# Optimization experiments

Hardware: AMD Instinct MI355X
Metric: run time of the kernel (lower is better)

Reference implementation:

```python
import jax, jax.numpy as jnp
import numpy as np

B, W, F = 32, 100, 128   # batch, window_size, n_features
KSIZE = 7                # conv kernel size
EMB = 8                  # embedding dim for feature-similarity matrix
ALPHA = 0.2              # leaky relu negative slope


def setup_inputs() -> dict:
    key = jax.random.key(0)
    ks = jax.random.split(key, 10)
    s = 0.05
    return {
        "x": jax.random.normal(ks[0], (B, W, F), jnp.float32),
        # ConvLayer: Conv1d(F, F, KSIZE) with 'same' padding
        "conv_w": jax.random.normal(ks[1], (F, F, KSIZE), jnp.float32) * s,
        "conv_b": jnp.zeros((F,), jnp.float32),
        # TemporalAttentionLayer (GATv2): lin(2F -> 2F), a (2F,1), bias (W,W)
        "temp_lin_w": jax.random.normal(ks[2], (2 * F, 2 * F), jnp.float32) * s,
        "temp_lin_b": jnp.zeros((2 * F,), jnp.float32),
        "temp_a": jax.random.normal(ks[3], (2 * F, 1), jnp.float32) * s,
        "temp_bias": jnp.zeros((W, W), jnp.float32),
        # FeatureAttentionLayer (GATv2): lin(2W -> 2W), a (2W,1), bias (F,F)
        "feat_lin_w": jax.random.normal(ks[4], (2 * W, 2 * W), jnp.float32) * s,
        "feat_lin_b": jnp.zeros((2 * W,), jnp.float32),
        "feat_a": jax.random.normal(ks[5], (2 * W, 1), jnp.float32) * s,
        "feat_bias": jnp.zeros((F, F), jnp.float32),
        # nn.Embedding(F, EMB) table (indexed by arange(F) -> just the table)
        "emb": jax.random.normal(ks[6], (F, EMB), jnp.float32),
        # forecasting model: Linear(W, 1) + tanh
        "fc_w": jax.random.normal(ks[7], (1, W), jnp.float32) * s,
        "fc_b": jnp.zeros((1,), jnp.float32),
    }


def _pos_encode(x):
    # pe = sin(pos*div) + cos(pos*div), div = exp(arange(F) * -ln(1e4)/F)
    pos = jnp.arange(W, dtype=jnp.float32)[:, None]
    div = jnp.exp(jnp.arange(F, dtype=jnp.float32) * (-np.log(10000.0) / F))
    pe = jnp.sin(pos * div) + jnp.cos(pos * div)  # (W, F)
    return x + pe[None]


def _conv(x, w, b):
    # x: (B, W, F) -> Conv1d over time with channels = features, 'same' length
    xc = x.transpose(0, 2, 1)  # (B, F, W)
    pad = (KSIZE - 1) // 2
    y = jax.lax.conv_general_dilated(
        xc, w, window_strides=(1,), padding=[(pad, pad)],
        dimension_numbers=("NCW", "OIW", "NCW"))
    y = jax.nn.relu(y + b[None, :, None])
    return y.transpose(0, 2, 1)  # (B, W, F)


def _gat_v2(v, lin_w, lin_b, a, bias):
    # v: (B, K, D). Equivalent to lin(concat(v_i, v_j)) via split weights +
    # broadcast add (avoids the O(K^2) concat materialization).
    D = v.shape[-1]
    left = v @ lin_w[:, :D].T    # (B, K, E) -- v_i part
    right = v @ lin_w[:, D:].T   # (B, K, E) -- v_j part
    s = left[:, :, None, :] + right[:, None, :, :] + lin_b  # (B, K, K, E)
    s = jnp.where(s >= 0, s, ALPHA * s)  # leaky relu
    e = jnp.einsum("bije,e->bij", s, a[:, 0]) + bias  # (B, K, K)
    att = jax.nn.softmax(e, axis=2)
    return jnp.tanh(jnp.einsum("bij,bjd->bid", att, v))


def reference(x, conv_w, conv_b, temp_lin_w, temp_lin_b, temp_a, temp_bias,
              feat_lin_w, feat_lin_b, feat_a, feat_bias, emb, fc_w, fc_b):
    x = _pos_encode(x)                 # (B, W, F)
    x = _conv(x, conv_w, conv_b)       # (B, W, F)
    # temporal attention: nodes = time steps
    x = _gat_v2(x, temp_lin_w, temp_lin_b, temp_a, temp_bias)  # (B, W, F)
    # feature attention: nodes = features
    xf = x.transpose(0, 2, 1)          # (B, F, W)
    xf = _gat_v2(xf, feat_lin_w, feat_lin_b, feat_a, feat_bias)
    x = xf.transpose(0, 2, 1)          # (B, W, F)
    # cosine-similarity mixing over features
    norms = jnp.linalg.norm(emb, axis=-1)
    cos = (emb @ emb.T) / (norms[:, None] * norms[None, :])  # (F, F)
    x = x @ cos.T                      # (B, W, F)
    xp = x.transpose(0, 2, 1)          # (B, F, W)
    pred = jnp.tanh(xp @ fc_w.T + fc_b)  # (B, F, 1)
    return pred.transpose(0, 2, 1)     # (B, 1, F)
```

## Files before the change

### kernel.cpp

```cpp
#include <hip/hip_runtime.h>
#include <math.h>

#define BB 32
#define WW 100
#define FF 128
#define KS 7
#define ET 256
#define EF 200


__global__ void k_prep(const float* __restrict__ cw, const float* __restrict__ tlw,
                       const float* __restrict__ flw, float* __restrict__ wt,
                       float* __restrict__ tlwT, float* __restrict__ flwT) {
    int id = blockIdx.x * 256 + threadIdx.x;
    if (id < KS * FF * FF) {
        int o = id & (FF - 1);
        int r = id >> 7;
        int k = r % KS;
        int i = r / KS;
        wt[id] = cw[(o * FF + i) * KS + k];
    }
    if (id < ET * ET) {
        int e = id & (ET - 1);
        int d = id >> 8;
        tlwT[id] = tlw[e * ET + d];
    }
    if (id < EF * EF) {
        int e = id % EF;
        int d = id / EF;
        flwT[id] = flw[e * EF + d];
    }
}

#define CTW 10
#define NROW 16
#define XPAD 20
__global__ __launch_bounds__(512) void k_conv(const float* __restrict__ x,
                                              const float* __restrict__ wt,
                                              const float* __restrict__ cb,
                                              float* __restrict__ x2) {
    int b = blockIdx.x & 31;
    int tile = blockIdx.x >> 5;
    int w0 = tile * CTW;
    int tid = threadIdx.x;
    int o = tid & (FF - 1);
    int h = tid >> 7;
    __shared__ float xs[FF][XPAD];
    __shared__ float part[4][CTW][FF];
    for (int idx = tid; idx < NROW * FF; idx += 512) {
        int r = idx >> 7, f = idx & (FF - 1);
        int t = w0 - 3 + r;
        float v = 0.f;
        if ((unsigned)t < WW) {
            float div = __expf((float)f * (-9.210340371976184f / (float)FF));
            float arg = (float)t * div;
            v = x[(b * WW + t) * FF + f] + __sinf(arg) + __cosf(arg);
        }
        xs[f][r] = v;
    }
    __syncthreads();
    float acc[CTW];
#pragma unroll
    for (int t = 0; t < CTW; ++t) acc[t] = 0.f;
    const float* wbase = wt + (h * 32) * KS * FF + o;
#pragma unroll 2
    for (int il = 0; il < 32; ++il) {
        int i = h * 32 + il;
        float4 X0 = *(const float4*)&xs[i][0];
        float4 X1 = *(const float4*)&xs[i][4];
        float4 X2 = *(const float4*)&xs[i][8];
        float4 X3 = *(const float4*)&xs[i][12];
        float xr[16] = {X0.x, X0.y, X0.z, X0.w, X1.x, X1.y, X1.z, X1.w,
                        X2.x, X2.y, X2.z, X2.w, X3.x, X3.y, X3.z, X3.w};
        const float* wp = wbase + il * KS * FF;
#pragma unroll
        for (int k = 0; k < KS; ++k) {
            float wv = wp[k * FF];
#pragma unroll
            for (int t = 0; t < CTW; ++t) acc[t] += xr[t + k] * wv;
        }
    }
#pragma unroll
    for (int t = 0; t < CTW; ++t) part[h][t][o] = acc[t];
    __syncthreads();
    for (int idx = tid; idx < CTW * FF; idx += 512) {
        int t = idx >> 7, oo = idx & (FF - 1);
        float s = part[0][t][oo] + part[1][t][oo] + part[2][t][oo] +
                  part[3][t][oo] + cb[oo];
        x2[(b * WW + w0 + t) * FF + oo] = fmaxf(s, 0.f);
    }
}

__global__ __launch_bounds__(512) void k_lr_t(const float* __restrict__ x2,
                                              const float* __restrict__ tlwT,
                                              const float* __restrict__ tlb,
                                              float* __restrict__ LT,
                                              float* __restrict__ Rt) {
    int b = blockIdx.x & 31;
    int tile = blockIdx.x >> 5;
    int i0 = tile * 8;
    int tid = threadIdx.x;
    int e = tid & 255;
    int rh = tid >> 8;
    __shared__ float xs[8][FF];
    for (int idx = tid; idx < 8 * FF; idx += 512) {
        int r = idx >> 7, d = idx & (FF - 1);
        int row = i0 + r; if (row >= WW) row = WW - 1;
        xs[r][d] = x2[(b * WW + row) * FF + d];
    }
    __syncthreads();
    float aL[4] = {0, 0, 0, 0}, aR[4] = {0, 0, 0, 0};
    const float* wl = tlwT + e;
#pragma unroll 2
    for (int dc = 0; dc < 32; ++dc) {
        float xv[4][4];
#pragma unroll
        for (int r = 0; r < 4; ++r)
            *(float4*)xv[r] = *(const float4*)&xs[rh * 4 + r][dc * 4];
#pragma unroll
        for (int q = 0; q < 4; ++q) {
            int d = dc * 4 + q;
            float wL = wl[d * ET];
            float wR = wl[(FF + d) * ET];
#pragma unroll
            for (int r = 0; r < 4; ++r) {
                aL[r] += xv[r][q] * wL;
                aR[r] += xv[r][q] * wR;
            }
        }
    }
    int ibase = i0 + rh * 4;
    if (ibase < WW) {
        float lb = tlb[e];
        float o0[4];
#pragma unroll
        for (int r = 0; r < 4; ++r) o0[r] = aL[r] + lb;
        *(float4*)&LT[(b * ET + e) * WW + ibase] = *(float4*)o0;
        *(float4*)&Rt[(b * ET + e) * WW + ibase] = *(float4*)aR;
    }
}

__global__ __launch_bounds__(512) void k_att_t(const float* __restrict__ LT,
                                               const float* __restrict__ Rt,
                                               const float* __restrict__ ta,
                                               const float* __restrict__ tbias,
                                               const float* __restrict__ x2,
                                               float* __restrict__ x3T) {
    int b = blockIdx.x & 31;
    int tile = blockIdx.x >> 5;
    int i0 = tile * 8;
    int tid = threadIdx.x;
    int j = tid & 127, g = tid >> 7;
    __shared__ float Rs[2][32][FF];
    __shared__ float Ls[2][32][8];
    __shared__ float tas[ET];
    __shared__ float attQ[8][FF];
    __shared__ float ob[8][FF];
    __shared__ float redA[8][2], redB[8][2];
    if (tid < ET) tas[tid] = ta[tid];

    float rv[8];
    float lvr = 0.f;
    {
        const float* Rb = Rt + (b * ET) * WW;
#pragma unroll
        for (int it = 0; it < 8; ++it) {
            int idx = tid + it * 512;
            int er = idx >> 7, w = idx & 127;
            rv[it] = (w < WW) ? Rb[er * WW + w] : 0.f;
        }
        if (tid < 256) {
            int er = tid >> 3, qq = tid & 7;
            int row = i0 + qq; if (row >= WW) row = WW - 1;
            lvr = LT[(b * ET + er) * WW + row];
        }
    }
#pragma unroll
    for (int it = 0; it < 8; ++it) {
        int idx = tid + it * 512;
        Rs[0][idx >> 7][idx & 127] = rv[it];
    }
    if (tid < 256) Ls[0][tid >> 3][tid & 7] = lvr;
    __syncthreads();

    float s0 = 0.f, s1 = 0.f;
    for (int ch = 0; ch < 8; ++ch) {
        int buf = ch & 1;
        if (ch < 7) {
            int e0 = (ch + 1) * 32;
            const float* Rb = Rt + (b * ET + e0) * WW;
#pragma unroll
            for (int it = 0; it < 8; ++it) {
                int idx = tid + it * 512;
                int er = idx >> 7, w = idx & 127;
                rv[it] = (w < WW) ? Rb[er * WW + w] : 0.f;
            }
            if (tid < 256) {
                int er = tid >> 3, qq = tid & 7;
                int row = i0 + qq; if (row >= WW) row = WW - 1;
                lvr = LT[(b * ET + e0 + er) * WW + row];
            }
        }
        int e0 = ch * 32;
#pragma unroll 8
        for (int e = 0; e < 32; ++e) {
            float rj = Rs[buf][e][j];
            float ae = tas[e0 + e];
            float2 lv2 = *(const float2*)&Ls[buf][e][g * 2];
            float v;
            v = lv2.x + rj; v = fmaxf(v, 0.2f * v); s0 += v * ae;
            v = lv2.y + rj; v = fmaxf(v, 0.2f * v); s1 += v * ae;
        }
        if (ch < 7) {
#pragma unroll
            for (int it = 0; it < 8; ++it) {
                int idx = tid + it * 512;
                Rs[buf ^ 1][idx >> 7][idx & 127] = rv[it];
            }
            if (tid < 256) Ls[buf ^ 1][tid >> 3][tid & 7] = lvr;
        }
        __syncthreads();
    }

    float ej[2];
    {
        int iq = i0 + g * 2;
        float bv0 = (j < WW && iq < WW) ? tbias[iq * WW + j] : 0.f;
        float bv1 = (j < WW && iq + 1 < WW) ? tbias[(iq + 1) * WW + j] : 0.f;
        ej[0] = (j < WW && iq < WW) ? s0 + bv0 : -1e30f;
        ej[1] = (j < WW && iq + 1 < WW) ? s1 + bv1 : -1e30f;
    }
    float m[2] = {ej[0], ej[1]};
#pragma unroll
    for (int off = 32; off > 0; off >>= 1) {
#pragma unroll
        for (int ii = 0; ii < 2; ++ii) m[ii] = fmaxf(m[ii], __shfl_xor(m[ii], off));
    }
    int wv = tid >> 6;
    if ((tid & 63) == 0) { redA[wv][0] = m[0]; redA[wv][1] = m[1]; }
    __syncthreads();
    float p[2], ps[2];
#pragma unroll
    for (int ii = 0; ii < 2; ++ii) {
        float mx = fmaxf(redA[g * 2][ii], redA[g * 2 + 1][ii]);
        p[ii] = (j < WW) ? __expf(ej[ii] - mx) : 0.f;
        ps[ii] = p[ii];
    }
#pragma unroll
    for (int off = 32; off > 0; off >>= 1) {
#pragma unroll
        for (int ii = 0; ii < 2; ++ii) ps[ii] += __shfl_xor(ps[ii], off);
    }
    if ((tid & 63) == 0) { redB[wv][0] = ps[0]; redB[wv][1] = ps[1]; }
    __syncthreads();
#pragma unroll
    for (int ii = 0; ii < 2; ++ii) {
        float inv = 1.f / (redB[g * 2][ii] + redB[g * 2 + 1][ii]);
        attQ[g * 2 + ii][j] = p[ii] * inv;
    }

    int d = j, ph = g;
    float pv0 = 0.f, pv1 = 0.f;
#pragma unroll
    for (int it = 0; it < 8; ++it) {
        int idx = tid + it * 512;
        int r = idx >> 7, f = idx & 127;
        rv[it] = (r < WW) ? x2[(b * WW + r) * FF + f] : 0.f;
    }
    __syncthreads();
#pragma unroll
    for (int it = 0; it < 8; ++it) {
        int idx = tid + it * 512;
        Rs[0][idx >> 7][idx & 127] = rv[it];
    }
    __syncthreads();
    const float* a0 = attQ[ph * 2];
    const float* a1 = attQ[ph * 2 + 1];
    for (int jc = 0; jc < 4; ++jc) {
        int buf = jc & 1;
        if (jc < 3) {
            int r0 = (jc + 1) * 32;
#pragma unroll
            for (int it = 0; it < 8; ++it) {
                int idx = tid + it * 512;
                int r = idx >> 7, f = idx & 127;
                int row = r0 + r;
                rv[it] = (row < WW) ? x2[(b * WW + row) * FF + f] : 0.f;
            }
        }
#pragma unroll 8
        for (int r = 0; r < 32; ++r) {
            float xv = Rs[buf][r][d];
            int row = jc * 32 + r;
            pv0 += a0[row] * xv;
            pv1 += a1[row] * xv;
        }
        if (jc < 3) {
#pragma unroll
            for (int it = 0; it < 8; ++it) {
                int idx = tid + it * 512;
                Rs[buf ^ 1][idx >> 7][idx & 127] = rv[it];
            }
        }
        __syncthreads();
    }
    ob[ph * 2][d] = tanhf(pv0);
    ob[ph * 2 + 1][d] = tanhf(pv1);
    __syncthreads();
    if (tid < 256) {
        int f = tid >> 1, half = tid & 1;
        if (i0 + half * 4 < WW) {
            float4 v = make_float4(ob[half * 4][f], ob[half * 4 + 1][f],
                                   ob[half * 4 + 2][f], ob[half * 4 + 3][f]);
            *(float4*)&x3T[(b * FF + f) * WW + i0 + half * 4] = v;
        }
    }
}

__global__ __launch_bounds__(512) void k_lr_f(const float* __restrict__ x3T,
                                              const float* __restrict__ flwT,
                                              const float* __restrict__ flb,
                                              float* __restrict__ LfT,
                                              float* __restrict__ RfT) {
    int b = blockIdx.x & 31;
    int tile = blockIdx.x >> 5;
    int f0 = tile * 8;
    int tid = threadIdx.x;
    int e = tid & 255;
    int rh = tid >> 8;
    __shared__ float xs[8][WW];
    for (int idx = tid; idx < 8 * WW; idx += 512) {
        int r = idx / WW, d = idx % WW;
        xs[r][d] = x3T[(b * FF + f0 + r) * WW + d];
    }
    __syncthreads();
    if (e < EF) {
        float aL[4] = {0, 0, 0, 0}, aR[4] = {0, 0, 0, 0};
        const float* wl = flwT + e;
#pragma unroll 2
        for (int dc = 0; dc < 25; ++dc) {
            float xv[4][4];
#pragma unroll
            for (int r = 0; r < 4; ++r)
                *(float4*)xv[r] = *(const float4*)&xs[rh * 4 + r][dc * 4];
#pragma unroll
            for (int q = 0; q < 4; ++q) {
                int d = dc * 4 + q;
                float wL = wl[d * EF];
                float wR = wl[(WW + d) * EF];
#pragma unroll
                for (int r = 0; r < 4; ++r) {
                    aL[r] += xv[r][q] * wL;
                    aR[r] += xv[r][q] * wR;
                }
            }
        }
        float lb = flb[e];
        float o0[4];
#pragma unroll
        for (int r = 0; r < 4; ++r) o0[r] = aL[r] + lb;
        int fbase = f0 + rh * 4;
        *(float4*)&LfT[(b * EF + e) * FF + fbase] = *(float4*)o0;
        *(float4*)&RfT[(b * EF + e) * FF + fbase] = *(float4*)aR;
    }
}

__global__ __launch_bounds__(512) void k_att_f(const float* __restrict__ LfT,
                                               const float* __restrict__ RfT,
                                               const float* __restrict__ fa,
                                               const float* __restrict__ fbias,
                                               const float* __restrict__ x3T,
                                               const float* __restrict__ fcw,
                                               float* __restrict__ tj) {
    int b = blockIdx.x & 31;
    int tile = blockIdx.x >> 5;
    int f0 = tile * 8;
    int tid = threadIdx.x;
    int j = tid & 127, g = tid >> 7;
    __shared__ float Rs[2][40][FF];
    __shared__ float Ls[2][40][8];
    __shared__ float fas[EF];
    __shared__ float attQ[8][FF];
    __shared__ float redA[8][2], redB[8][2], redT[8][2];
    if (tid < EF) fas[tid] = fa[tid];

    float rv[10];
    float lvr = 0.f;
    {
        const float* Rb = RfT + (b * EF) * FF;
#pragma unroll
        for (int it = 0; it < 10; ++it) {
            int idx = tid + it * 512;
            rv[it] = Rb[idx];
        }
        if (tid < 320) {
            int er = tid >> 3, qq = tid & 7;
            lvr = LfT[(b * EF + er) * FF + f0 + qq];
        }
    }
#pragma unroll
    for (int it = 0; it < 10; ++it) {
        int idx = tid + it * 512;
        Rs[0][idx >> 7][idx & 127] = rv[it];
    }
    if (tid < 320) Ls[0][tid >> 3][tid & 7] = lvr;
    __syncthreads();

    float s0 = 0.f, s1 = 0.f;
    for (int ch = 0; ch < 5; ++ch) {
        int buf = ch & 1;
        if (ch < 4) {
            int e0 = (ch + 1) * 40;
            const float* Rb = RfT + (b * EF + e0) * FF;
#pragma unroll
            for (int it = 0; it < 10; ++it) {
                int idx = tid + it * 512;
                rv[it] = Rb[idx];
            }
            if (tid < 320) {
                int er = tid >> 3, qq = tid & 7;
                lvr = LfT[(b * EF + e0 + er) * FF + f0 + qq];
            }
        }
        int e0 = ch * 40;
#pragma unroll 8
        for (int e = 0; e < 40; ++e) {
            float rj = Rs[buf][e][j];
            float ae = fas[e0 + e];
            float2 lv2 = *(const float2*)&Ls[buf][e][g * 2];
            float v;
            v = lv2.x + rj; v = fmaxf(v, 0.2f * v); s0 += v * ae;
            v = lv2.y + rj; v = fmaxf(v, 0.2f * v); s1 += v * ae;
        }
        if (ch < 4) {
#pragma unroll
            for (int it = 0; it < 10; ++it) {
                int idx = tid + it * 512;
                Rs[buf ^ 1][idx >> 7][idx & 127] = rv[it];
            }
            if (tid < 320) Ls[buf ^ 1][tid >> 3][tid & 7] = lvr;
        }
        __syncthreads();
    }

    float ej[2] = {s0 + fbias[(f0 + g * 2) * FF + j],
                   s1 + fbias[(f0 + g * 2 + 1) * FF + j]};
    float m[2] = {ej[0], ej[1]};
#pragma unroll
    for (int off = 32; off > 0; off >>= 1) {
#pragma unroll
        for (int ii = 0; ii < 2; ++ii) m[ii] = fmaxf(m[ii], __shfl_xor(m[ii], off));
    }
    int wv = tid >> 6;
    if ((tid & 63) == 0) { redA[wv][0] = m[0]; redA[wv][1] = m[1]; }
    __syncthreads();
    float p[2], ps[2];
#pragma unroll
    for (int ii = 0; ii < 2; ++ii) {
        float mx = fmaxf(redA[g * 2][ii], redA[g * 2 + 1][ii]);
        p[ii] = __expf(ej[ii] - mx);
        ps[ii] = p[ii];
    }
#pragma unroll
    for (int off = 32; off > 0; off >>= 1) {
#pragma unroll
        for (int ii = 0; ii < 2; ++ii) ps[ii] += __shfl_xor(ps[ii], off);
    }
    if ((tid & 63) == 0) { redB[wv][0] = ps[0]; redB[wv][1] = ps[1]; }
    __syncthreads();
#pragma unroll
    for (int ii = 0; ii < 2; ++ii) {
        float inv = 1.f / (redB[g * 2][ii] + redB[g * 2 + 1][ii]);
        attQ[g * 2 + ii][j] = p[ii] * inv;
    }

    int w = j, ph = g;
    float pv0 = 0.f, pv1 = 0.f;
#pragma unroll
    for (int it = 0; it < 8; ++it) {
        int idx = tid + it * 512;
        int r = idx >> 7, ww = idx & 127;
        rv[it] = (ww < WW) ? x3T[(b * FF + r) * WW + ww] : 0.f;
    }
    __syncthreads();
#pragma unroll
    for (int it = 0; it < 8; ++it) {
        int idx = tid + it * 512;
        Rs[0][idx >> 7][idx & 127] = rv[it];
    }
    __syncthreads();
    const float* a0 = attQ[ph * 2];
    const float* a1 = attQ[ph * 2 + 1];
    for (int jc = 0; jc < 4; ++jc) {
        int buf = jc & 1;
        if (jc < 3) {
            int r0 = (jc + 1) * 32;
#pragma unroll
            for (int it = 0; it < 8; ++it) {
                int idx = tid + it * 512;
                int r = idx >> 7, ww = idx & 127;
                rv[it] = (ww < WW) ? x3T[(b * FF + r0 + r) * WW + ww] : 0.f;
            }
        }
#pragma unroll 8
        for (int r = 0; r < 32; ++r) {
            float xv = Rs[buf][r][w];
            int row = jc * 32 + r;
            pv0 += a0[row] * xv;
            pv1 += a1[row] * xv;
        }
        if (jc < 3) {
#pragma unroll
            for (int it = 0; it < 8; ++it) {
                int idx = tid + it * 512;
                Rs[buf ^ 1][idx >> 7][idx & 127] = rv[it];
            }
        }
        __syncthreads();
    }
    bool wok = (w < WW);
    float fcv = wok ? fcw[w] : 0.f;
    float tv[2] = {tanhf(pv0) * fcv, tanhf(pv1) * fcv};
#pragma unroll
    for (int off = 32; off > 0; off >>= 1) {
#pragma unroll
        for (int ii = 0; ii < 2; ++ii) tv[ii] += __shfl_xor(tv[ii], off);
    }
    if ((tid & 63) == 0) { redT[wv][0] = tv[0]; redT[wv][1] = tv[1]; }
    __syncthreads();
    if (tid < 8) {
        int q = tid, php = q >> 1, ii = q & 1;
        tj[b * FF + f0 + q] = redT[php * 2][ii] + redT[php * 2 + 1][ii];
    }
}

__global__ __launch_bounds__(128) void k_fc(const float* __restrict__ tjg,
                                            const float* __restrict__ emb,
                                            const float* __restrict__ fcb,
                                            float* __restrict__ out) {
    int b = blockIdx.x;
    int f = threadIdx.x;
    __shared__ float en[FF][12];
    __shared__ float tjs[FF];
    {
        float4 e0 = *(const float4*)&emb[f * 8];
        float4 e1 = *(const float4*)&emb[f * 8 + 4];
        float n = e0.x*e0.x + e0.y*e0.y + e0.z*e0.z + e0.w*e0.w +
                  e1.x*e1.x + e1.y*e1.y + e1.z*e1.z + e1.w*e1.w;
        float rin = rsqrtf(n);
        float4 a = make_float4(e0.x*rin, e0.y*rin, e0.z*rin, e0.w*rin);
        float4 c = make_float4(e1.x*rin, e1.y*rin, e1.z*rin, e1.w*rin);
        *(float4*)&en[f][0] = a;
        *(float4*)&en[f][4] = c;
        tjs[f] = tjg[b * FF + f];
    }
    __syncthreads();
    float er[8];
#pragma unroll
    for (int k = 0; k < 8; ++k) er[k] = en[f][k];
    float acc = fcb[0];
    for (int jj = 0; jj < FF; ++jj) {
        float4 a = *(const float4*)&en[jj][0];
        float4 c = *(const float4*)&en[jj][4];
        float d8 = er[0]*a.x + er[1]*a.y + er[2]*a.z + er[3]*a.w +
                   er[4]*c.x + er[5]*c.y + er[6]*c.z + er[7]*c.w;
        acc += d8 * tjs[jj];
    }
    out[b * FF + f] = tanhf(acc);
}

extern "C" void kernel_launch(void* const* d_in, const int* in_sizes, int n_in,
                              void* d_out, int out_size, void* d_ws, size_t ws_size,
                              hipStream_t stream) {
    const float* x     = (const float*)d_in[0];
    const float* cw    = (const float*)d_in[1];
    const float* cb    = (const float*)d_in[2];
    const float* tlw   = (const float*)d_in[3];
    const float* tlb   = (const float*)d_in[4];
    const float* ta    = (const float*)d_in[5];
    const float* tbias = (const float*)d_in[6];
    const float* flw   = (const float*)d_in[7];
    const float* flb   = (const float*)d_in[8];
    const float* fa    = (const float*)d_in[9];
    const float* fbias = (const float*)d_in[10];
    const float* emb   = (const float*)d_in[11];
    const float* fcw   = (const float*)d_in[12];
    const float* fcb   = (const float*)d_in[13];
    float* out = (float*)d_out;
    float* ws = (float*)d_ws;

    float* x2   = ws + 409600;
    float* x3T  = ws + 819200;
    float* LT   = ws + 1228800;
    float* Rt   = ws + 2048000;
    float* tj   = ws + 2867200;
    float* wt   = ws + 3297280;
    float* tlwT = ws + 3411968;
    float* flwT = ws + 3477504;

    k_prep<<<448, 256, 0, stream>>>(cw, tlw, flw, wt, tlwT, flwT);
    k_conv<<<BB * 10, 512, 0, stream>>>(x, wt, cb, x2);
    k_lr_t<<<BB * 13, 512, 0, stream>>>(x2, tlwT, tlb, LT, Rt);
    k_att_t<<<BB * 13, 512, 0, stream>>>(LT, Rt, ta, tbias, x2, x3T);
    k_lr_f<<<BB * 16, 512, 0, stream>>>(x3T, flwT, flb, LT, Rt);
    k_att_f<<<BB * 16, 512, 0, stream>>>(LT, Rt, fa, fbias, x3T, fcw, tj);
    k_fc<<<BB, 128, 0, stream>>>(tj, emb, fcb, out);
}
```

Baseline: 118.2 us.

## Fuse temporal linear projection into conv and final FC into feature attention

The temporal GAT linear projection (L/R) is computed inside the conv kernel from the conv output held in shared memory, so the separate k_lr_t launch and its reload of x2 go away. The final cosine-mixing FC step moves into k_att_f: an atomic per-batch counter, reset in k_prep, picks the last finishing block for each batch, and that block computes the output. This saves two kernel launches and some global traffic. In exchange the conv kernel does more work per block at 320 blocks, and the result relies on threadfence/atomic ordering.

```diff
diff --git a/kernel.cpp b/kernel.cpp
--- a/kernel.cpp
+++ b/kernel.cpp
@@ -11,8 +11,10 @@
 
 __global__ void k_prep(const float* __restrict__ cw, const float* __restrict__ tlw,
                        const float* __restrict__ flw, float* __restrict__ wt,
-                       float* __restrict__ tlwT, float* __restrict__ flwT) {
+                       float* __restrict__ tlwT, float* __restrict__ flwT,
+                       int* __restrict__ cnt) {
     int id = blockIdx.x * 256 + threadIdx.x;
+    if (id < 32) cnt[id] = 0;
     if (id < KS * FF * FF) {
         int o = id & (FF - 1);
         int r = id >> 7;
@@ -38,7 +40,11 @@
 __global__ __launch_bounds__(512) void k_conv(const float* __restrict__ x,
                                               const float* __restrict__ wt,
                                               const float* __restrict__ cb,
-                                              float* __restrict__ x2) {
+                                              const float* __restrict__ tlwT,
+                                              const float* __restrict__ tlb,
+                                              float* __restrict__ x2,
+                                              float* __restrict__ LT,
+                                              float* __restrict__ Rt) {
     int b = blockIdx.x & 31;
     int tile = blockIdx.x >> 5;
     int w0 = tile * CTW;
@@ -47,6 +53,7 @@
     int h = tid >> 7;
     __shared__ float xs[FF][XPAD];
     __shared__ float part[4][CTW][FF];
+    __shared__ float xs2[CTW][FF];
     for (int idx = tid; idx < NROW * FF; idx += 512) {
         int r = idx >> 7, f = idx & (FF - 1);
         int t = w0 - 3 + r;
@@ -87,56 +94,41 @@
         int t = idx >> 7, oo = idx & (FF - 1);
         float s = part[0][t][oo] + part[1][t][oo] + part[2][t][oo] +
                   part[3][t][oo] + cb[oo];
-        x2[(b * WW + w0 + t) * FF + oo] = fmaxf(s, 0.f);
-    }
-}
-
-__global__ __launch_bounds__(512) void k_lr_t(const float* __restrict__ x2,
-                                              const float* __restrict__ tlwT,
-                                              const float* __restrict__ tlb,
-                                              float* __restrict__ LT,
-                                              float* __restrict__ Rt) {
-    int b = blockIdx.x & 31;
-    int tile = blockIdx.x >> 5;
-    int i0 = tile * 8;
-    int tid = threadIdx.x;
+        s = fmaxf(s, 0.f);
+        x2[(b * WW + w0 + t) * FF + oo] = s;
+        xs2[t][oo] = s;
+    }
+    __syncthreads();
     int e = tid & 255;
     int rh = tid >> 8;
-    __shared__ float xs[8][FF];
-    for (int idx = tid; idx < 8 * FF; idx += 512) {
-        int r = idx >> 7, d = idx & (FF - 1);
-        int row = i0 + r; if (row >= WW) row = WW - 1;
-        xs[r][d] = x2[(b * WW + row) * FF + d];
-    }
-    __syncthreads();
-    float aL[4] = {0, 0, 0, 0}, aR[4] = {0, 0, 0, 0};
+    float aL[5] = {0, 0, 0, 0, 0}, aR[5] = {0, 0, 0, 0, 0};
     const float* wl = tlwT + e;
 #pragma unroll 2
     for (int dc = 0; dc < 32; ++dc) {
-        float xv[4][4];
-#pragma unroll
-        for (int r = 0; r < 4; ++r)
-            *(float4*)xv[r] = *(const float4*)&xs[rh * 4 + r][dc * 4];
+        float xv[5][4];
+#pragma unroll
+        for (int r = 0; r < 5; ++r)
+            *(float4*)xv[r] = *(const float4*)&xs2[rh * 5 + r][dc * 4];
 #pragma unroll
         for (int q = 0; q < 4; ++q) {
             int d = dc * 4 + q;
             float wL = wl[d * ET];
             float wR = wl[(FF + d) * ET];
 #pragma unroll
-            for (int r = 0; r < 4; ++r) {
+            for (int r = 0; r < 5; ++r) {
                 aL[r] += xv[r][q] * wL;
                 aR[r] += xv[r][q] * wR;
             }
         }
     }
-    int ibase = i0 + rh * 4;
-    if (ibase < WW) {
-        float lb = tlb[e];
-        float o0[4];
-#pragma unroll
-        for (int r = 0; r < 4; ++r) o0[r] = aL[r] + lb;
-        *(float4*)&LT[(b * ET + e) * WW + ibase] = *(float4*)o0;
-        *(float4*)&Rt[(b * ET + e) * WW + ibase] = *(float4*)aR;
+    float lb = tlb[e];
+    int ibase = w0 + rh * 5;
+    float* Lp = LT + (b * ET + e) * WW + ibase;
+    float* Rp = Rt + (b * ET + e) * WW + ibase;
+#pragma unroll
+    for (int r = 0; r < 5; ++r) {
+        Lp[r] = aL[r] + lb;
+        Rp[r] = aR[r];
     }
 }
 
@@ -371,7 +363,11 @@
                                                const float* __restrict__ fbias,
                                                const float* __restrict__ x3T,
                                                const float* __restrict__ fcw,
-                                               float* __restrict__ tj) {
+                                               const float* __restrict__ emb,
+                                               const float* __restrict__ fcb,
+                                               float* __restrict__ tj,
+                                               int* __restrict__ cnt,
+                                               float* __restrict__ out) {
     int b = blockIdx.x & 31;
     int tile = blockIdx.x >> 5;
     int f0 = tile * 8;
@@ -382,6 +378,9 @@
     __shared__ float fas[EF];
     __shared__ float attQ[8][FF];
     __shared__ float redA[8][2], redB[8][2], redT[8][2];
+    __shared__ float en[FF][12];
+    __shared__ float tjs2[FF];
+    __shared__ int isLast;
     if (tid < EF) fas[tid] = fa[tid];
 
     float rv[10];
@@ -532,41 +531,45 @@
         int q = tid, php = q >> 1, ii = q & 1;
         tj[b * FF + f0 + q] = redT[php * 2][ii] + redT[php * 2 + 1][ii];
     }
-}
-
-__global__ __launch_bounds__(128) void k_fc(const float* __restrict__ tjg,
-                                            const float* __restrict__ emb,
-                                            const float* __restrict__ fcb,
-                                            float* __restrict__ out) {
-    int b = blockIdx.x;
-    int f = threadIdx.x;
-    __shared__ float en[FF][12];
-    __shared__ float tjs[FF];
-    {
-        float4 e0 = *(const float4*)&emb[f * 8];
-        float4 e1 = *(const float4*)&emb[f * 8 + 4];
-        float n = e0.x*e0.x + e0.y*e0.y + e0.z*e0.z + e0.w*e0.w +
-                  e1.x*e1.x + e1.y*e1.y + e1.z*e1.z + e1.w*e1.w;
-        float rin = rsqrtf(n);
-        float4 a = make_float4(e0.x*rin, e0.y*rin, e0.z*rin, e0.w*rin);
-        float4 c = make_float4(e1.x*rin, e1.y*rin, e1.z*rin, e1.w*rin);
-        *(float4*)&en[f][0] = a;
-        *(float4*)&en[f][4] = c;
-        tjs[f] = tjg[b * FF + f];
-    }
-    __syncthreads();
-    float er[8];
-#pragma unroll
-    for (int k = 0; k < 8; ++k) er[k] = en[f][k];
-    float acc = fcb[0];
-    for (int jj = 0; jj < FF; ++jj) {
-        float4 a = *(const float4*)&en[jj][0];
-        float4 c = *(const float4*)&en[jj][4];
-        float d8 = er[0]*a.x + er[1]*a.y + er[2]*a.z + er[3]*a.w +
-                   er[4]*c.x + er[5]*c.y + er[6]*c.z + er[7]*c.w;
-        acc += d8 * tjs[jj];
-    }
-    out[b * FF + f] = tanhf(acc);
+    __syncthreads();
+    if (tid == 0) {
+        __threadfence();
+        int old = atomicAdd(&cnt[b], 1);
+        isLast = (old == 15);
+    }
+    __syncthreads();
+    if (isLast) {
+        __threadfence();
+        if (tid < 128) {
+            int f = tid;
+            float4 e0 = *(const float4*)&emb[f * 8];
+            float4 e1 = *(const float4*)&emb[f * 8 + 4];
+            float n = e0.x*e0.x + e0.y*e0.y + e0.z*e0.z + e0.w*e0.w +
+                      e1.x*e1.x + e1.y*e1.y + e1.z*e1.z + e1.w*e1.w;
+            float rin = rsqrtf(n);
+            en[f][0] = e0.x*rin; en[f][1] = e0.y*rin;
+            en[f][2] = e0.z*rin; en[f][3] = e0.w*rin;
+            en[f][4] = e1.x*rin; en[f][5] = e1.y*rin;
+            en[f][6] = e1.z*rin; en[f][7] = e1.w*rin;
+            tjs2[f] = tj[b * FF + f];
+        }
+        __syncthreads();
+        if (tid < 128) {
+            int f = tid;
+            float er[8];
+#pragma unroll
+            for (int k = 0; k < 8; ++k) er[k] = en[f][k];
+            float acc = fcb[0];
+            for (int jj = 0; jj < FF; ++jj) {
+                float4 a = *(const float4*)&en[jj][0];
+                float4 c = *(const float4*)&en[jj][4];
+                float d8 = er[0]*a.x + er[1]*a.y + er[2]*a.z + er[3]*a.w +
+                           er[4]*c.x + er[5]*c.y + er[6]*c.z + er[7]*c.w;
+                acc += d8 * tjs2[jj];
+            }
+            out[b * FF + f] = tanhf(acc);
+        }
+    }
 }
 
 extern "C" void kernel_launch(void* const* d_in, const int* in_sizes, int n_in,
@@ -594,15 +597,15 @@
     float* LT   = ws + 1228800;
     float* Rt   = ws + 2048000;
     float* tj   = ws + 2867200;
+    int*   cnt  = (int*)(ws + 2871296);
     float* wt   = ws + 3297280;
     float* tlwT = ws + 3411968;
     float* flwT = ws + 3477504;
 
-    k_prep<<<448, 256, 0, stream>>>(cw, tlw, flw, wt, tlwT, flwT);
-    k_conv<<<BB * 10, 512, 0, stream>>>(x, wt, cb, x2);
-    k_lr_t<<<BB * 13, 512, 0, stream>>>(x2, tlwT, tlb, LT, Rt);
+    k_prep<<<448, 256, 0, stream>>>(cw, tlw, flw, wt, tlwT, flwT, cnt);
+    k_conv<<<BB * 10, 512, 0, stream>>>(x, wt, cb, tlwT, tlb, x2, LT, Rt);
     k_att_t<<<BB * 13, 512, 0, stream>>>(LT, Rt, ta, tbias, x2, x3T);
     k_lr_f<<<BB * 16, 512, 0, stream>>>(x3T, flwT, flb, LT, Rt);
-    k_att_f<<<BB * 16, 512, 0, stream>>>(LT, Rt, fa, fbias, x3T, fcw, tj);
-    k_fc<<<BB, 128, 0, stream>>>(tj, emb, fcb, out);
+    k_att_f<<<BB * 16, 512, 0, stream>>>(LT, Rt, fa, fbias, x3T, fcw,
+                                         emb, fcb, tj, cnt, out);
 }
```

Measured after the change: 123.6 us. 4.6% more time.

## Split attention reductions across thread groups with four query rows per thread

Applied to the files above, without the earlier changes.

In both the temporal and feature attention kernels, each thread now accumulates four query rows instead of two, reading them with a float4 from the shared L tile. Half the threads cover each half of the embedding (and of the value rows), and the two partial sums are combined through a shared buffer. This raises reuse of each Rs/xv shared-memory load across more rows and shrinks per-row shared reads. The cost is an extra shared-memory reduction, an extra barrier, and half the threads sitting idle during the softmax and output stages.

```diff
diff --git a/kernel.cpp b/kernel.cpp
--- a/kernel.cpp
+++ b/kernel.cpp
@@ -150,13 +150,16 @@
     int tile = blockIdx.x >> 5;
     int i0 = tile * 8;
     int tid = threadIdx.x;
-    int j = tid & 127, g = tid >> 7;
+    int j = tid & 127;
+    int u = tid >> 7;
+    int qh = u & 1;
+    int eh = u >> 1;
     __shared__ float Rs[2][32][FF];
     __shared__ float Ls[2][32][8];
     __shared__ float tas[ET];
-    __shared__ float attQ[8][FF];
-    __shared__ float ob[8][FF];
-    __shared__ float redA[8][2], redB[8][2];
+    __shared__ float sacc[8][FF];
+    __shared__ float attQT[FF][8];
+    __shared__ float redA[8][4], redB[8][4];
     if (tid < ET) tas[tid] = ta[tid];
 
     float rv[8];
@@ -183,12 +186,12 @@
     if (tid < 256) Ls[0][tid >> 3][tid & 7] = lvr;
     __syncthreads();
 
-    float s0 = 0.f, s1 = 0.f;
+    float s[4] = {0.f, 0.f, 0.f, 0.f};
     for (int ch = 0; ch < 8; ++ch) {
         int buf = ch & 1;
         if (ch < 7) {
-            int e0 = (ch + 1) * 32;
-            const float* Rb = Rt + (b * ET + e0) * WW;
+            int e0n = (ch + 1) * 32;
+            const float* Rb = Rt + (b * ET + e0n) * WW;
 #pragma unroll
             for (int it = 0; it < 8; ++it) {
                 int idx = tid + it * 512;
@@ -198,18 +201,21 @@
             if (tid < 256) {
                 int er = tid >> 3, qq = tid & 7;
                 int row = i0 + qq; if (row >= WW) row = WW - 1;
-                lvr = LT[(b * ET + e0 + er) * WW + row];
+                lvr = LT[(b * ET + e0n + er) * WW + row];
             }
         }
         int e0 = ch * 32;
-#pragma unroll 8
-        for (int e = 0; e < 32; ++e) {
+#pragma unroll
+        for (int el = 0; el < 16; ++el) {
+            int e = eh * 16 + el;
             float rj = Rs[buf][e][j];
             float ae = tas[e0 + e];
-            float2 lv2 = *(const float2*)&Ls[buf][e][g * 2];
+            float4 lv = *(const float4*)&Ls[buf][e][qh * 4];
             float v;
-            v = lv2.x + rj; v = fmaxf(v, 0.2f * v); s0 += v * ae;
-            v = lv2.y + rj; v = fmaxf(v, 0.2f * v); s1 += v * ae;
+            v = lv.x + rj; v = fmaxf(v, 0.2f * v); s[0] += v * ae;
+            v = lv.y + rj; v = fmaxf(v, 0.2f * v); s[1] += v * ae;
+            v = lv.z + rj; v = fmaxf(v, 0.2f * v); s[2] += v * ae;
+            v = lv.w + rj; v = fmaxf(v, 0.2f * v); s[3] += v * ae;
         }
         if (ch < 7) {
 #pragma unroll
@@ -221,46 +227,63 @@
         }
         __syncthreads();
     }
-
-    float ej[2];
-    {
-        int iq = i0 + g * 2;
-        float bv0 = (j < WW && iq < WW) ? tbias[iq * WW + j] : 0.f;
-        float bv1 = (j < WW && iq + 1 < WW) ? tbias[(iq + 1) * WW + j] : 0.f;
-        ej[0] = (j < WW && iq < WW) ? s0 + bv0 : -1e30f;
-        ej[1] = (j < WW && iq + 1 < WW) ? s1 + bv1 : -1e30f;
-    }
-    float m[2] = {ej[0], ej[1]};
+    if (eh == 1) {
+#pragma unroll
+        for (int c = 0; c < 4; ++c) sacc[qh * 4 + c][j] = s[c];
+    }
+    __syncthreads();
+    float ej[4], p[4];
+    if (eh == 0) {
+#pragma unroll
+        for (int c = 0; c < 4; ++c) {
+            int i = i0 + qh * 4 + c;
+            float v = s[c] + sacc[qh * 4 + c][j];
+            v += (j < WW && i < WW) ? tbias[i * WW + j] : 0.f;
+            ej[c] = (j < WW && i < WW) ? v : -1e30f;
+        }
+    } else {
+#pragma unroll
+        for (int c = 0; c < 4; ++c) ej[c] = -1e30f;
+    }
+    float m[4] = {ej[0], ej[1], ej[2], ej[3]};
 #pragma unroll
     for (int off = 32; off > 0; off >>= 1) {
 #pragma unroll
-        for (int ii = 0; ii < 2; ++ii) m[ii] = fmaxf(m[ii], __shfl_xor(m[ii], off));
+        for (int c = 0; c < 4; ++c) m[c] = fmaxf(m[c], __shfl_xor(m[c], off));
     }
     int wv = tid >> 6;
-    if ((tid & 63) == 0) { redA[wv][0] = m[0]; redA[wv][1] = m[1]; }
-    __syncthreads();
-    float p[2], ps[2];
-#pragma unroll
-    for (int ii = 0; ii < 2; ++ii) {
-        float mx = fmaxf(redA[g * 2][ii], redA[g * 2 + 1][ii]);
-        p[ii] = (j < WW) ? __expf(ej[ii] - mx) : 0.f;
-        ps[ii] = p[ii];
+    if ((tid & 63) == 0) {
+#pragma unroll
+        for (int c = 0; c < 4; ++c) redA[wv][c] = m[c];
+    }
+    __syncthreads();
+    float ps[4];
+#pragma unroll
+    for (int c = 0; c < 4; ++c) {
+        float mx = fmaxf(redA[wv][c], redA[wv ^ 1][c]);
+        p[c] = (eh == 0 && j < WW) ? __expf(ej[c] - mx) : 0.f;
+        ps[c] = p[c];
     }
 #pragma unroll
     for (int off = 32; off > 0; off >>= 1) {
 #pragma unroll
-        for (int ii = 0; ii < 2; ++ii) ps[ii] += __shfl_xor(ps[ii], off);
-    }
-    if ((tid & 63) == 0) { redB[wv][0] = ps[0]; redB[wv][1] = ps[1]; }
-    __syncthreads();
-#pragma unroll
-    for (int ii = 0; ii < 2; ++ii) {
-        float inv = 1.f / (redB[g * 2][ii] + redB[g * 2 + 1][ii]);
-        attQ[g * 2 + ii][j] = p[ii] * inv;
-    }
-
-    int d = j, ph = g;
-    float pv0 = 0.f, pv1 = 0.f;
+        for (int c = 0; c < 4; ++c) ps[c] += __shfl_xor(ps[c], off);
+    }
+    if ((tid & 63) == 0) {
+#pragma unroll
+        for (int c = 0; c < 4; ++c) redB[wv][c] = ps[c];
+    }
+    __syncthreads();
+    if (eh == 0) {
+#pragma unroll
+        for (int c = 0; c < 4; ++c) {
+            float inv = 1.f / (redB[wv][c] + redB[wv ^ 1][c]);
+            attQT[j][qh * 4 + c] = p[c] * inv;
+        }
+    }
+
+    int d = j, qq = qh, rh = eh;
+    float pv[4] = {0.f, 0.f, 0.f, 0.f};
 #pragma unroll
     for (int it = 0; it < 8; ++it) {
         int idx = tid + it * 512;
@@ -274,8 +297,6 @@
         Rs[0][idx >> 7][idx & 127] = rv[it];
     }
     __syncthreads();
-    const float* a0 = attQ[ph * 2];
-    const float* a1 = attQ[ph * 2 + 1];
     for (int jc = 0; jc < 4; ++jc) {
         int buf = jc & 1;
         if (jc < 3) {
@@ -288,12 +309,13 @@
                 rv[it] = (row < WW) ? x2[(b * WW + row) * FF + f] : 0.f;
             }
         }
-#pragma unroll 8
-        for (int r = 0; r < 32; ++r) {
+#pragma unroll
+        for (int rr = 0; rr < 16; ++rr) {
+            int r = rh * 16 + rr;
             float xv = Rs[buf][r][d];
-            int row = jc * 32 + r;
-            pv0 += a0[row] * xv;
-            pv1 += a1[row] * xv;
+            float4 av = *(const float4*)&attQT[jc * 32 + r][qq * 4];
+            pv[0] += av.x * xv; pv[1] += av.y * xv;
+            pv[2] += av.z * xv; pv[3] += av.w * xv;
         }
         if (jc < 3) {
 #pragma unroll
@@ -304,16 +326,17 @@
         }
         __syncthreads();
     }
-    ob[ph * 2][d] = tanhf(pv0);
-    ob[ph * 2 + 1][d] = tanhf(pv1);
-    __syncthreads();
-    if (tid < 256) {
-        int f = tid >> 1, half = tid & 1;
-        if (i0 + half * 4 < WW) {
-            float4 v = make_float4(ob[half * 4][f], ob[half * 4 + 1][f],
-                                   ob[half * 4 + 2][f], ob[half * 4 + 3][f]);
-            *(float4*)&x3T[(b * FF + f) * WW + i0 + half * 4] = v;
-        }
+    if (rh == 1) {
+#pragma unroll
+        for (int c = 0; c < 4; ++c) sacc[qq * 4 + c][d] = pv[c];
+    }
+    __syncthreads();
+    if (rh == 0) {
+        float o0[4];
+#pragma unroll
+        for (int c = 0; c < 4; ++c) o0[c] = tanhf(pv[c] + sacc[qq * 4 + c][d]);
+        if (i0 + qq * 4 < WW)
+            *(float4*)&x3T[(b * FF + d) * WW + i0 + qq * 4] = *(float4*)o0;
     }
 }
 
@@ -376,12 +399,16 @@
     int tile = blockIdx.x >> 5;
     int f0 = tile * 8;
     int tid = threadIdx.x;
-    int j = tid & 127, g = tid >> 7;
+    int j = tid & 127;
+    int u = tid >> 7;
+    int qh = u & 1;
+    int eh = u >> 1;
     __shared__ float Rs[2][40][FF];
     __shared__ float Ls[2][40][8];
     __shared__ float fas[EF];
-    __shared__ float attQ[8][FF];
-    __shared__ float redA[8][2], redB[8][2], redT[8][2];
+    __shared__ float sacc[8][FF];
+    __shared__ float attQT[FF][8];
+    __shared__ float redA[8][4], redB[8][4], redT[8][4];
     if (tid < EF) fas[tid] = fa[tid];
 
     float rv[10];
@@ -406,12 +433,12 @@
     if (tid < 320) Ls[0][tid >> 3][tid & 7] = lvr;
     __syncthreads();
 
-    float s0 = 0.f, s1 = 0.f;
+    float s[4] = {0.f, 0.f, 0.f, 0.f};
     for (int ch = 0; ch < 5; ++ch) {
         int buf = ch & 1;
         if (ch < 4) {
-            int e0 = (ch + 1) * 40;
-            const float* Rb = RfT + (b * EF + e0) * FF;
+            int e0n = (ch + 1) * 40;
+            const float* Rb = RfT + (b * EF + e0n) * FF;
 #pragma unroll
             for (int it = 0; it < 10; ++it) {
                 int idx = tid + it * 512;
@@ -419,18 +446,21 @@
             }
             if (tid < 320) {
                 int er = tid >> 3, qq = tid & 7;
-                lvr = LfT[(b * EF + e0 + er) * FF + f0 + qq];
+                lvr = LfT[(b * EF + e0n + er) * FF + f0 + qq];
             }
         }
         int e0 = ch * 40;
-#pragma unroll 8
-        for (int e = 0; e < 40; ++e) {
+#pragma unroll
+        for (int el = 0; el < 20; ++el) {
+            int e = eh * 20 + el;
             float rj = Rs[buf][e][j];
             float ae = fas[e0 + e];
-            float2 lv2 = *(const float2*)&Ls[buf][e][g * 2];
+            float4 lv = *(const float4*)&Ls[buf][e][qh * 4];
             float v;
-            v = lv2.x + rj; v = fmaxf(v, 0.2f * v); s0 += v * ae;
-            v = lv2.y + rj; v = fmaxf(v, 0.2f * v); s1 += v * ae;
+            v = lv.x + rj; v = fmaxf(v, 0.2f * v); s[0] += v * ae;
+            v = lv.y + rj; v = fmaxf(v, 0.2f * v); s[1] += v * ae;
+            v = lv.z + rj; v = fmaxf(v, 0.2f * v); s[2] += v * ae;
+            v = lv.w + rj; v = fmaxf(v, 0.2f * v); s[3] += v * ae;
         }
         if (ch < 4) {
 #pragma unroll
@@ -442,40 +472,59 @@
         }
         __syncthreads();
     }
-
-    float ej[2] = {s0 + fbias[(f0 + g * 2) * FF + j],
-                   s1 + fbias[(f0 + g * 2 + 1) * FF + j]};
-    float m[2] = {ej[0], ej[1]};
+    if (eh == 1) {
+#pragma unroll
+        for (int c = 0; c < 4; ++c) sacc[qh * 4 + c][j] = s[c];
+    }
+    __syncthreads();
+    float ej[4], p[4];
+    if (eh == 0) {
+#pragma unroll
+        for (int c = 0; c < 4; ++c)
+            ej[c] = s[c] + sacc[qh * 4 + c][j] + fbias[(f0 + qh * 4 + c) * FF + j];
+    } else {
+#pragma unroll
+        for (int c = 0; c < 4; ++c) ej[c] = -1e30f;
+    }
+    float m[4] = {ej[0], ej[1], ej[2], ej[3]};
 #pragma unroll
     for (int off = 32; off > 0; off >>= 1) {
 #pragma unroll
-        for (int ii = 0; ii < 2; ++ii) m[ii] = fmaxf(m[ii], __shfl_xor(m[ii], off));
+        for (int c = 0; c < 4; ++c) m[c] = fmaxf(m[c], __shfl_xor(m[c], off));
     }
     int wv = tid >> 6;
-    if ((tid & 63) == 0) { redA[wv][0] = m[0]; redA[wv][1] = m[1]; }
-    __syncthreads();
-    float p[2], ps[2];
-#pragma unroll
-    for (int ii = 0; ii < 2; ++ii) {
-        float mx = fmaxf(redA[g * 2][ii], redA[g * 2 + 1][ii]);
-        p[ii] = __expf(ej[ii] - mx);
-        ps[ii] = p[ii];
+    if ((tid & 63) == 0) {
+#pragma unroll
+        for (int c = 0; c < 4; ++c) redA[wv][c] = m[c];
+    }
+    __syncthreads();
+    float ps[4];
+#pragma unroll
+    for (int c = 0; c < 4; ++c) {
+        float mx = fmaxf(redA[wv][c], redA[wv ^ 1][c]);
+        p[c] = (eh == 0) ? __expf(ej[c] - mx) : 0.f;
+        ps[c] = p[c];
     }
 #pragma unroll
     for (int off = 32; off > 0; off >>= 1) {
 #pragma unroll
-        for (int ii = 0; ii < 2; ++ii) ps[ii] += __shfl_xor(ps[ii], off);
-    }
-    if ((tid & 63) == 0) { redB[wv][0] = ps[0]; redB[wv][1] = ps[1]; }
-    __syncthreads();
-#pragma unroll
-    for (int ii = 0; ii < 2; ++ii) {
-        float inv = 1.f / (redB[g * 2][ii] + redB[g * 2 + 1][ii]);
-        attQ[g * 2 + ii][j] = p[ii] * inv;
-    }
-
-    int w = j, ph = g;
-    float pv0 = 0.f, pv1 = 0.f;
+        for (int c = 0; c < 4; ++c) ps[c] += __shfl_xor(ps[c], off);
+    }
+    if ((tid & 63) == 0) {
+#pragma unroll
+        for (int c = 0; c < 4; ++c) redB[wv][c] = ps[c];
+    }
+    __syncthreads();
+    if (eh == 0) {
+#pragma unroll
+        for (int c = 0; c < 4; ++c) {
+            float inv = 1.f / (redB[wv][c] + redB[wv ^ 1][c]);
+            attQT[j][qh * 4 + c] = p[c] * inv;
+        }
+    }
+
+    int w = j, qq = qh, rh = eh;
+    float pv[4] = {0.f, 0.f, 0.f, 0.f};
 #pragma unroll
     for (int it = 0; it < 8; ++it) {
         int idx = tid + it * 512;
@@ -489,8 +538,6 @@
         Rs[0][idx >> 7][idx & 127] = rv[it];
     }
     __syncthreads();
-    const float* a0 = attQ[ph * 2];
-    const float* a1 = attQ[ph * 2 + 1];
     for (int jc = 0; jc < 4; ++jc) {
         int buf = jc & 1;
         if (jc < 3) {
@@ -502,12 +549,13 @@
                 rv[it] = (ww < WW) ? x3T[(b * FF + r0 + r) * WW + ww] : 0.f;
             }
         }
-#pragma unroll 8
-        for (int r = 0; r < 32; ++r) {
+#pragma unroll
+        for (int rr = 0; rr < 16; ++rr) {
+            int r = rh * 16 + rr;
             float xv = Rs[buf][r][w];
-            int row = jc * 32 + r;
-            pv0 += a0[row] * xv;
-            pv1 += a1[row] * xv;
+            float4 av = *(const float4*)&attQT[jc * 32 + r][qq * 4];
+            pv[0] += av.x * xv; pv[1] += av.y * xv;
+            pv[2] += av.z * xv; pv[3] += av.w * xv;
         }
         if (jc < 3) {
 #pragma unroll
@@ -518,19 +566,32 @@
         }
         __syncthreads();
     }
-    bool wok = (w < WW);
-    float fcv = wok ? fcw[w] : 0.f;
-    float tv[2] = {tanhf(pv0) * fcv, tanhf(pv1) * fcv};
-#pragma unroll
-    for (int off = 32; off > 0; off >>= 1) {
-#pragma unroll
-        for (int ii = 0; ii < 2; ++ii) tv[ii] += __shfl_xor(tv[ii], off);
-    }
-    if ((tid & 63) == 0) { redT[wv][0] = tv[0]; redT[wv][1] = tv[1]; }
+    if (rh == 1) {
+#pragma unroll
+        for (int c = 0; c < 4; ++c) sacc[qq * 4 + c][w] = pv[c];
+    }
+    __syncthreads();
+    if (rh == 0) {
+        bool wok = (w < WW);
+        float fcv = wok ? fcw[w] : 0.f;
+        float tv[4];
+#pragma unroll
+        for (int c = 0; c < 4; ++c)
+            tv[c] = tanhf(pv[c] + sacc[qq * 4 + c][w]) * fcv;
+#pragma unroll
+        for (int off = 32; off > 0; off >>= 1) {
+#pragma unroll
+            for (int c = 0; c < 4; ++c) tv[c] += __shfl_xor(tv[c], off);
+        }
+        if ((tid & 63) == 0) {
+#pragma unroll
+            for (int c = 0; c < 4; ++c) redT[wv][c] = tv[c];
+        }
+    }
     __syncthreads();
     if (tid < 8) {
-        int q = tid, php = q >> 1, ii = q & 1;
-        tj[b * FF + f0 + q] = redT[php * 2][ii] + redT[php * 2 + 1][ii];
+        int q = tid, qqo = q >> 2, c = q & 3;
+        tj[b * FF + f0 + q] = redT[qqo * 2][c] + redT[qqo * 2 + 1][c];
     }
 }
 
```

Measured after the change: 130.2 us. +10.1%, slower.
